# Optimization experiments

Hardware: AMD Instinct MI355X
Metric: run time of the kernel (lower is better)

Reference implementation:

```python
import jax, jax.numpy as jnp
import numpy as np

B, N, IN_F, H, F = 2, 4096, 256, 4, 64
NEG_INF = -9e15


def setup_inputs() -> dict:
    key = jax.random.key(0)
    k_x, k_w, k_as, k_ad, k_adj = jax.random.split(key, 5)
    x = jax.random.normal(k_x, (B, N, IN_F), dtype=jnp.float32)
    # torch Linear weight: (out_features*H, in_features)
    W = jax.random.normal(k_w, (H * F, IN_F), dtype=jnp.float32) * (1.0 / np.sqrt(IN_F))
    # a_src/a_dst stored as (H, F) == original (1, H, F) squeezed
    gain = 1.414
    bound = gain * np.sqrt(6.0 / (H * F + 1))
    a_src = jax.random.uniform(k_as, (H, F), jnp.float32, -bound, bound)
    a_dst = jax.random.uniform(k_ad, (H, F), jnp.float32, -bound, bound)
    up = jax.random.bernoulli(k_adj, 0.01, (N, N)).astype(jnp.float32)
    adj = jnp.clip(up + up.T + jnp.eye(N, dtype=jnp.float32), 0.0, 1.0)
    return {"x": x, "adj": adj, "W": W, "a_src": a_src, "a_dst": a_dst}


def reference(x, adj, W, a_src, a_dst):
    # h: [B, N, H, F]
    h = (x @ W.T).reshape(B, N, H, F)
    s_src = jnp.einsum("bnhf,hf->bnh", h, a_src)  # [B,N,H]
    s_dst = jnp.einsum("bnhf,hf->bnh", h, a_dst)  # [B,N,H]
    # e: [B, N(dst rows), M(src/neighbor), H]
    e = s_src[:, :, None, :] + s_dst[:, None, :, :]
    e = jax.nn.leaky_relu(e, 0.2)
    mask = (adj > 0)[None, :, :, None]  # [1,N,N,1]
    e = jnp.where(mask, e, NEG_INF)
    attn = jax.nn.softmax(e, axis=2)  # softmax over neighbor dim m
    h_prime = jnp.einsum("bnmh,bmhf->bnhf", attn, h)
    return h_prime.reshape(B, N, H * F)
```

## Files before the change

### kernel.cpp

```cpp
#include <hip/hip_runtime.h>
#include <hip/hip_bf16.h>

#define B_ 2
#define N_ 4096
#define INF_ 256
#define H_ 4
#define F_ 64
#define HF_ 256
#define MAXN 256
#define MAXNP 257

typedef __bf16 bf16x8 __attribute__((ext_vector_type(8)));
typedef float f32x4 __attribute__((ext_vector_type(4)));
typedef ushort u16x8 __attribute__((ext_vector_type(8)));

__device__ inline float bfbits2f(ushort u) {
  union { uint i; float f; } v; v.i = ((uint)u) << 16; return v.f;
}

__global__ __launch_bounds__(256) void gemm_h_kernel(const float* __restrict__ x,
                                                     const float* __restrict__ W,
                                                     const float* __restrict__ a_src,
                                                     const float* __restrict__ a_dst,
                                                     __hip_bfloat16* __restrict__ hout,
                                                     float* __restrict__ s_src,
                                                     float* __restrict__ s_dst) {
  const int wave = threadIdx.x >> 6;
  const int lane = threadIdx.x & 63;
  const int m0 = (blockIdx.x * 4 + wave) * 16;
  const int head = blockIdx.y;
  const int nb = head * 64;
  const int r16 = lane & 15;
  const int q = lane >> 4;

  const float* ap = x + (size_t)(m0 + r16) * INF_ + q * 8;
  bf16x8 afrag[8];
#pragma unroll
  for (int kk = 0; kk < 8; ++kk) {
    f32x4 a0 = *(const f32x4*)(ap + kk * 32);
    f32x4 a1 = *(const f32x4*)(ap + kk * 32 + 4);
#pragma unroll
    for (int i = 0; i < 4; ++i) {
      afrag[kk][i] = (__bf16)a0[i];
      afrag[kk][4 + i] = (__bf16)a1[i];
    }
  }

  f32x4 acc4[4];
#pragma unroll
  for (int tile = 0; tile < 4; ++tile) {
    const int n0 = nb + tile * 16;
    const float* bp = W + (size_t)(n0 + r16) * INF_ + q * 8;
    f32x4 acc = {0.f, 0.f, 0.f, 0.f};
#pragma unroll
    for (int kk = 0; kk < 8; ++kk) {
      f32x4 b0 = *(const f32x4*)(bp + kk * 32);
      f32x4 b1 = *(const f32x4*)(bp + kk * 32 + 4);
      bf16x8 bv;
#pragma unroll
      for (int i = 0; i < 4; ++i) {
        bv[i] = (__bf16)b0[i];
        bv[4 + i] = (__bf16)b1[i];
      }
      acc = __builtin_amdgcn_mfma_f32_16x16x32_bf16(afrag[kk], bv, acc, 0, 0, 0);
    }
    acc4[tile] = acc;
  }

#pragma unroll
  for (int tile = 0; tile < 4; ++tile) {
#pragma unroll
    for (int r = 0; r < 4; ++r) {
      hout[(size_t)(m0 + q * 4 + r) * HF_ + nb + tile * 16 + r16] =
          __float2bfloat16(acc4[tile][r]);
    }
  }

  float ps[4] = {0.f, 0.f, 0.f, 0.f}, pd[4] = {0.f, 0.f, 0.f, 0.f};
#pragma unroll
  for (int tile = 0; tile < 4; ++tile) {
    const float asv = a_src[nb + tile * 16 + r16];
    const float adv = a_dst[nb + tile * 16 + r16];
#pragma unroll
    for (int r = 0; r < 4; ++r) {
      ps[r] += acc4[tile][r] * asv;
      pd[r] += acc4[tile][r] * adv;
    }
  }
#pragma unroll
  for (int off = 1; off < 16; off <<= 1) {
#pragma unroll
    for (int r = 0; r < 4; ++r) {
      ps[r] += __shfl_xor(ps[r], off);
      pd[r] += __shfl_xor(pd[r], off);
    }
  }
  if (r16 == 0) {
#pragma unroll
    for (int r = 0; r < 4; ++r) {
      s_src[(size_t)(m0 + q * 4 + r) * H_ + head] = ps[r];
      s_dst[(size_t)(m0 + q * 4 + r) * H_ + head] = pd[r];
    }
  }
}

__global__ __launch_bounds__(512) void attn_kernel(const uint* __restrict__ adj,
                                                   const __hip_bfloat16* __restrict__ hmat,
                                                   const float* __restrict__ s_src,
                                                   const float* __restrict__ s_dst,
                                                   float* __restrict__ out) {
  const int n = blockIdx.x;
  const int t = threadIdx.x;
  const int wv = t >> 6, lane = t & 63;
  const int b = wv >> 2, hh = wv & 3;
  __shared__ int cnt;
  __shared__ int nidx[MAXN];
  __shared__ float ev[2 * H_ * MAXNP];
  __shared__ float ssrc_sh[2 * H_];
  if (t == 0) cnt = 0;
  __syncthreads();

  const uint4* arow = (const uint4*)(adj + (size_t)n * N_);
  for (int i = t; i < N_ / 4; i += 512) {
    const uint4 v = arow[i];
    const int base = i * 4;
    int p;
    if (v.x) { p = atomicAdd(&cnt, 1); if (p < MAXN) nidx[p] = base; }
    if (v.y) { p = atomicAdd(&cnt, 1); if (p < MAXN) nidx[p] = base + 1; }
    if (v.z) { p = atomicAdd(&cnt, 1); if (p < MAXN) nidx[p] = base + 2; }
    if (v.w) { p = atomicAdd(&cnt, 1); if (p < MAXN) nidx[p] = base + 3; }
  }
  if (t < 2 * H_) ssrc_sh[t] = s_src[((size_t)(t >> 2) * N_ + n) * H_ + (t & 3)];
  __syncthreads();
  const int C = (cnt < MAXN) ? cnt : MAXN;

  for (int u = t; u < C * 8; u += 512) {
    const int j = u >> 3, sub = u & 7, b2 = sub >> 2, h2 = sub & 3;
    float e = ssrc_sh[sub] + s_dst[((size_t)b2 * N_ + nidx[j]) * H_ + h2];
    e = (e > 0.f) ? e : 0.2f * e;
    ev[sub * MAXNP + j] = e;
  }
  __syncthreads();

  float* evw = ev + wv * MAXNP;
  float mx = -3.0e38f;
  for (int j = lane; j < C; j += 64) mx = fmaxf(mx, evw[j]);
#pragma unroll
  for (int off = 32; off > 0; off >>= 1) mx = fmaxf(mx, __shfl_xor(mx, off));
  float sum = 0.f;
  for (int j = lane; j < C; j += 64) sum += __expf(evw[j] - mx);
#pragma unroll
  for (int off = 32; off > 0; off >>= 1) sum += __shfl_xor(sum, off);
  const float inv = 1.f / sum;
  for (int j = lane; j < C; j += 64) evw[j] = __expf(evw[j] - mx) * inv;
  __syncthreads();

  const ushort* hb = (const ushort*)hmat + (size_t)b * N_ * HF_;
  const int jq = lane >> 3, f8 = lane & 7;
  float acc[8] = {0.f, 0.f, 0.f, 0.f, 0.f, 0.f, 0.f, 0.f};
#pragma unroll 2
  for (int j0 = 0; j0 < C; j0 += 8) {
    const int j = j0 + jq;
    if (j < C) {
      const float w = evw[j];
      const u16x8 v = *(const u16x8*)(hb + (size_t)nidx[j] * HF_ + hh * F_ + f8 * 8);
#pragma unroll
      for (int i = 0; i < 8; ++i) acc[i] += w * bfbits2f(v[i]);
    }
  }
#pragma unroll
  for (int off = 8; off < 64; off <<= 1) {
#pragma unroll
    for (int i = 0; i < 8; ++i) acc[i] += __shfl_xor(acc[i], off);
  }
  if (lane < 8) {
    float* op = out + ((size_t)b * N_ + n) * HF_ + hh * F_ + lane * 8;
    *(f32x4*)op = *(f32x4*)&acc[0];
    *(f32x4*)(op + 4) = *(f32x4*)&acc[4];
  }
}

extern "C" void kernel_launch(void* const* d_in, const int* in_sizes, int n_in,
                              void* d_out, int out_size, void* d_ws, size_t ws_size,
                              hipStream_t stream) {
  const float *xp = nullptr, *adjp = nullptr, *Wp = nullptr;
  const float *a3 = nullptr, *a4 = nullptr;
  for (int i = 0; i < n_in; ++i) {
    const int s = in_sizes[i];
    const float* p = (const float*)d_in[i];
    if (s == B_ * N_ * INF_) xp = p;
    else if (s == N_ * N_) adjp = p;
    else if (s == HF_ * INF_) Wp = p;
    else if (s == H_ * F_) { if (!a3) a3 = p; else a4 = p; }
  }
  if (!xp || !adjp || !Wp || !a3 || !a4) {
    xp = (const float*)d_in[0]; adjp = (const float*)d_in[1];
    Wp = (const float*)d_in[2]; a3 = (const float*)d_in[3]; a4 = (const float*)d_in[4];
  }
  float* out = (float*)d_out;

  __hip_bfloat16* h_ws = (__hip_bfloat16*)d_ws;
  float* s_src = (float*)((char*)d_ws + (size_t)B_ * N_ * HF_ * sizeof(__hip_bfloat16));
  float* s_dst = s_src + (size_t)B_ * N_ * H_;

  gemm_h_kernel<<<dim3(B_ * N_ / 64, H_), 256, 0, stream>>>(xp, Wp, a3, a4, h_ws, s_src, s_dst);
  attn_kernel<<<dim3(N_), 512, 0, stream>>>((const uint*)adjp, h_ws, s_src, s_dst, out);
}
```

Measured before the change: 155.9 us.

## Stage GEMM operands in LDS and process two heads per wave in attention

The projection GEMM now loads a 64-row tile of x and W into shared memory as bf16 once per block, so the four waves no longer each re-read and convert the same W tile from global memory. The attention kernel drops to 256 threads with each wave handling two heads. Softmax normalisation is deferred to the output, which removes a pass over the scores and the barrier before aggregation. Fewer waves per row means less parallelism for hiding latency on the gather loads, and the GEMM adds about 66KB of LDS per block.

```diff
diff --git a/kernel.cpp b/kernel.cpp
--- a/kernel.cpp
+++ b/kernel.cpp
@@ -9,6 +9,7 @@
 #define HF_ 256
 #define MAXN 256
 #define MAXNP 257
+#define XST 264
 
 typedef __bf16 bf16x8 __attribute__((ext_vector_type(8)));
 typedef float f32x4 __attribute__((ext_vector_type(4)));
@@ -25,53 +26,50 @@
                                                      __hip_bfloat16* __restrict__ hout,
                                                      float* __restrict__ s_src,
                                                      float* __restrict__ s_dst) {
-  const int wave = threadIdx.x >> 6;
-  const int lane = threadIdx.x & 63;
-  const int m0 = (blockIdx.x * 4 + wave) * 16;
-  const int head = blockIdx.y;
-  const int nb = head * 64;
-  const int r16 = lane & 15;
-  const int q = lane >> 4;
-
-  const float* ap = x + (size_t)(m0 + r16) * INF_ + q * 8;
+  __shared__ __bf16 xs[64 * XST];
+  __shared__ __bf16 wsh[64 * XST];
+  const int t = threadIdx.x;
+  const int wv = t >> 6, lane = t & 63;
+  const int m0 = blockIdx.x * 64;
+  const int head = blockIdx.y, nb = head * 64;
+
+#pragma unroll 4
+  for (int p = 0; p < 16; ++p) {
+    const int row = p * 4 + wv;
+    f32x4 vx = *(const f32x4*)(x + (size_t)(m0 + row) * INF_ + lane * 4);
+    f32x4 vw = *(const f32x4*)(W + (size_t)(nb + row) * INF_ + lane * 4);
+    __bf16* dx = xs + row * XST + lane * 4;
+    __bf16* dw = wsh + row * XST + lane * 4;
+#pragma unroll
+    for (int i = 0; i < 4; ++i) { dx[i] = (__bf16)vx[i]; dw[i] = (__bf16)vw[i]; }
+  }
+  __syncthreads();
+
+  const int r16 = lane & 15, q = lane >> 4;
+  const __bf16* arow = xs + (wv * 16 + r16) * XST + q * 8;
   bf16x8 afrag[8];
 #pragma unroll
-  for (int kk = 0; kk < 8; ++kk) {
-    f32x4 a0 = *(const f32x4*)(ap + kk * 32);
-    f32x4 a1 = *(const f32x4*)(ap + kk * 32 + 4);
-#pragma unroll
-    for (int i = 0; i < 4; ++i) {
-      afrag[kk][i] = (__bf16)a0[i];
-      afrag[kk][4 + i] = (__bf16)a1[i];
-    }
-  }
+  for (int kk = 0; kk < 8; ++kk) afrag[kk] = *(const bf16x8*)(arow + kk * 32);
 
   f32x4 acc4[4];
 #pragma unroll
   for (int tile = 0; tile < 4; ++tile) {
-    const int n0 = nb + tile * 16;
-    const float* bp = W + (size_t)(n0 + r16) * INF_ + q * 8;
+    const __bf16* brow = wsh + (tile * 16 + r16) * XST + q * 8;
     f32x4 acc = {0.f, 0.f, 0.f, 0.f};
 #pragma unroll
     for (int kk = 0; kk < 8; ++kk) {
-      f32x4 b0 = *(const f32x4*)(bp + kk * 32);
-      f32x4 b1 = *(const f32x4*)(bp + kk * 32 + 4);
-      bf16x8 bv;
-#pragma unroll
-      for (int i = 0; i < 4; ++i) {
-        bv[i] = (__bf16)b0[i];
-        bv[4 + i] = (__bf16)b1[i];
-      }
-      acc = __builtin_amdgcn_mfma_f32_16x16x32_bf16(afrag[kk], bv, acc, 0, 0, 0);
+      acc = __builtin_amdgcn_mfma_f32_16x16x32_bf16(
+          afrag[kk], *(const bf16x8*)(brow + kk * 32), acc, 0, 0, 0);
     }
     acc4[tile] = acc;
   }
 
+  const int m0w = m0 + wv * 16;
 #pragma unroll
   for (int tile = 0; tile < 4; ++tile) {
 #pragma unroll
     for (int r = 0; r < 4; ++r) {
-      hout[(size_t)(m0 + q * 4 + r) * HF_ + nb + tile * 16 + r16] =
+      hout[(size_t)(m0w + q * 4 + r) * HF_ + nb + tile * 16 + r16] =
           __float2bfloat16(acc4[tile][r]);
     }
   }
@@ -98,13 +96,13 @@
   if (r16 == 0) {
 #pragma unroll
     for (int r = 0; r < 4; ++r) {
-      s_src[(size_t)(m0 + q * 4 + r) * H_ + head] = ps[r];
-      s_dst[(size_t)(m0 + q * 4 + r) * H_ + head] = pd[r];
-    }
-  }
-}
-
-__global__ __launch_bounds__(512) void attn_kernel(const uint* __restrict__ adj,
+      s_src[(size_t)(m0w + q * 4 + r) * H_ + head] = ps[r];
+      s_dst[(size_t)(m0w + q * 4 + r) * H_ + head] = pd[r];
+    }
+  }
+}
+
+__global__ __launch_bounds__(256) void attn_kernel(const uint* __restrict__ adj,
                                                    const __hip_bfloat16* __restrict__ hmat,
                                                    const float* __restrict__ s_src,
                                                    const float* __restrict__ s_dst,
@@ -112,7 +110,8 @@
   const int n = blockIdx.x;
   const int t = threadIdx.x;
   const int wv = t >> 6, lane = t & 63;
-  const int b = wv >> 2, hh = wv & 3;
+  const int b = wv >> 1;
+  const int h0 = (wv & 1) * 2;
   __shared__ int cnt;
   __shared__ int nidx[MAXN];
   __shared__ float ev[2 * H_ * MAXNP];
@@ -121,7 +120,7 @@
   __syncthreads();
 
   const uint4* arow = (const uint4*)(adj + (size_t)n * N_);
-  for (int i = t; i < N_ / 4; i += 512) {
+  for (int i = t; i < N_ / 4; i += 256) {
     const uint4 v = arow[i];
     const int base = i * 4;
     int p;
@@ -134,7 +133,7 @@
   __syncthreads();
   const int C = (cnt < MAXN) ? cnt : MAXN;
 
-  for (int u = t; u < C * 8; u += 512) {
+  for (int u = t; u < C * 8; u += 256) {
     const int j = u >> 3, sub = u & 7, b2 = sub >> 2, h2 = sub & 3;
     float e = ssrc_sh[sub] + s_dst[((size_t)b2 * N_ + nidx[j]) * H_ + h2];
     e = (e > 0.f) ? e : 0.2f * e;
@@ -142,41 +141,67 @@
   }
   __syncthreads();
 
-  float* evw = ev + wv * MAXNP;
-  float mx = -3.0e38f;
-  for (int j = lane; j < C; j += 64) mx = fmaxf(mx, evw[j]);
-#pragma unroll
-  for (int off = 32; off > 0; off >>= 1) mx = fmaxf(mx, __shfl_xor(mx, off));
-  float sum = 0.f;
-  for (int j = lane; j < C; j += 64) sum += __expf(evw[j] - mx);
-#pragma unroll
-  for (int off = 32; off > 0; off >>= 1) sum += __shfl_xor(sum, off);
-  const float inv = 1.f / sum;
-  for (int j = lane; j < C; j += 64) evw[j] = __expf(evw[j] - mx) * inv;
-  __syncthreads();
+  float* ev0 = ev + (b * 4 + h0) * MAXNP;
+  float* ev1 = ev0 + MAXNP;
+  float mx0 = -3.0e38f, mx1 = -3.0e38f;
+  for (int j = lane; j < C; j += 64) {
+    mx0 = fmaxf(mx0, ev0[j]);
+    mx1 = fmaxf(mx1, ev1[j]);
+  }
+#pragma unroll
+  for (int off = 32; off > 0; off >>= 1) {
+    mx0 = fmaxf(mx0, __shfl_xor(mx0, off));
+    mx1 = fmaxf(mx1, __shfl_xor(mx1, off));
+  }
+  float s0 = 0.f, s1 = 0.f;
+  for (int j = lane; j < C; j += 64) {
+    const float e0 = __expf(ev0[j] - mx0); ev0[j] = e0; s0 += e0;
+    const float e1 = __expf(ev1[j] - mx1); ev1[j] = e1; s1 += e1;
+  }
+#pragma unroll
+  for (int off = 32; off > 0; off >>= 1) {
+    s0 += __shfl_xor(s0, off);
+    s1 += __shfl_xor(s1, off);
+  }
+  const float inv0 = 1.f / s0, inv1 = 1.f / s1;
 
   const ushort* hb = (const ushort*)hmat + (size_t)b * N_ * HF_;
   const int jq = lane >> 3, f8 = lane & 7;
-  float acc[8] = {0.f, 0.f, 0.f, 0.f, 0.f, 0.f, 0.f, 0.f};
+  float a0[8] = {0.f, 0.f, 0.f, 0.f, 0.f, 0.f, 0.f, 0.f};
+  float a1[8] = {0.f, 0.f, 0.f, 0.f, 0.f, 0.f, 0.f, 0.f};
 #pragma unroll 2
   for (int j0 = 0; j0 < C; j0 += 8) {
     const int j = j0 + jq;
     if (j < C) {
-      const float w = evw[j];
-      const u16x8 v = *(const u16x8*)(hb + (size_t)nidx[j] * HF_ + hh * F_ + f8 * 8);
-#pragma unroll
-      for (int i = 0; i < 8; ++i) acc[i] += w * bfbits2f(v[i]);
+      const ushort* hr = hb + (size_t)nidx[j] * HF_ + h0 * F_ + f8 * 8;
+      const u16x8 v0 = *(const u16x8*)hr;
+      const u16x8 v1 = *(const u16x8*)(hr + F_);
+      const float w0 = ev0[j], w1 = ev1[j];
+#pragma unroll
+      for (int i = 0; i < 8; ++i) {
+        a0[i] += w0 * bfbits2f(v0[i]);
+        a1[i] += w1 * bfbits2f(v1[i]);
+      }
     }
   }
 #pragma unroll
   for (int off = 8; off < 64; off <<= 1) {
 #pragma unroll
-    for (int i = 0; i < 8; ++i) acc[i] += __shfl_xor(acc[i], off);
+    for (int i = 0; i < 8; ++i) {
+      a0[i] += __shfl_xor(a0[i], off);
+      a1[i] += __shfl_xor(a1[i], off);
+    }
   }
   if (lane < 8) {
-    float* op = out + ((size_t)b * N_ + n) * HF_ + hh * F_ + lane * 8;
-    *(f32x4*)op = *(f32x4*)&acc[0];
-    *(f32x4*)(op + 4) = *(f32x4*)&acc[4];
+    float* op = out + ((size_t)b * N_ + n) * HF_ + h0 * F_ + lane * 8;
+    f32x4 o00 = {a0[0] * inv0, a0[1] * inv0, a0[2] * inv0, a0[3] * inv0};
+    f32x4 o01 = {a0[4] * inv0, a0[5] * inv0, a0[6] * inv0, a0[7] * inv0};
+    f32x4 o10 = {a1[0] * inv1, a1[1] * inv1, a1[2] * inv1, a1[3] * inv1};
+    f32x4 o11 = {a1[4] * inv1, a1[5] * inv1, a1[6] * inv1, a1[7] * inv1};
+    *(f32x4*)op = o00;
+    *(f32x4*)(op + 4) = o01;
+    *(f32x4*)(op + F_) = o10;
+    *(f32x4*)(op + F_ + 4) = o11;
   }
 }
 
@@ -204,5 +229,5 @@
   float* s_dst = s_src + (size_t)B_ * N_ * H_;
 
   gemm_h_kernel<<<dim3(B_ * N_ / 64, H_), 256, 0, stream>>>(xp, Wp, a3, a4, h_ws, s_src, s_dst);
-  attn_kernel<<<dim3(N_), 512, 0, stream>>>((const uint*)adjp, h_ws, s_src, s_dst, out);
-}
+  attn_kernel<<<dim3(N_), 256, 0, stream>>>((const uint*)adjp, h_ws, s_src, s_dst, out);
+}
```

After: 136.0 us. 1.15x faster.
